# Performance work log

Hardware: AMD Instinct MI355X
Metric: run time of the kernel (lower is better)

Reference implementation:

```python
import jax, jax.numpy as jnp
import numpy as np

B, S, D, H = 32, 512, 512, 8
DF = D // H  # dim_feature = 64
NEG_INF = -1e32


def setup_inputs() -> dict:
    key = jax.random.key(0)
    ks = jax.random.split(key, 8)
    std = 1.0 / np.sqrt(D)  # xavier-ish scale for square linears
    return {
        "q": jax.random.normal(ks[0], (B, S, D), jnp.float32),
        "k": jax.random.normal(ks[1], (B, S, D), jnp.float32),
        "v": jax.random.normal(ks[2], (B, S, D), jnp.float32),
        "mask": jnp.tril(jnp.ones((S, S), jnp.int32))[None, None],  # causal AKT mask
        "zero_pad": 1,
        "question_difficulty_emb": jax.random.normal(ks[3], (B, S, S), jnp.float32) * 0.1,
        "Wk": jax.random.normal(ks[4], (D, D), jnp.float32) * std,
        "bk": jnp.zeros((D,), jnp.float32),
        "Wv": jax.random.normal(ks[5], (D, D), jnp.float32) * std,
        "bv": jnp.zeros((D,), jnp.float32),
        "Wo": jax.random.normal(ks[6], (D, D), jnp.float32) * std,
        "bo": jnp.zeros((D,), jnp.float32),
        "gammas": jax.random.normal(ks[7], (H, 1, 1), jnp.float32) * 0.1,
    }


def reference(q, k, v, mask, zero_pad, question_difficulty_emb, Wk, bk, Wv, bv, Wo, bo, gammas):
    bs = q.shape[0]

    def proj(x, W, b):
        # Linear then split heads: [B,S,D] -> [B,H,S,DF]
        return (x @ W.T + b).reshape(bs, -1, H, DF).transpose(0, 2, 1, 3)

    qh = proj(q, Wk, bk)  # key_query_same=True: q uses key_linear
    kh = proj(k, Wk, bk)
    vh = proj(v, Wv, bv)

    scores = jnp.einsum("bhqd,bhkd->bhqk", qh, kh) / jnp.sqrt(jnp.float32(DF))
    seqlen = scores.shape[-1]
    maskb = mask == 0  # [1,1,S,S]

    # --- distance-decay term (computed under no_grad in torch, detached) ---
    scores_ = jax.nn.softmax(jnp.where(maskb, NEG_INF, scores), axis=-1)
    scores_ = scores_ * mask.astype(scores.dtype)
    distcum = jnp.cumsum(scores_, axis=-1)                      # [B,H,S,S]
    disttot = jnp.sum(scores_, axis=-1, keepdims=True)          # [B,H,S,1]
    pos = jnp.abs(jnp.arange(seqlen)[None, :] - jnp.arange(seqlen)[:, None]).astype(scores.dtype)
    dist_scores = jnp.sqrt(jnp.clip((disttot - distcum) * pos[None, None], 0.0))
    dist_scores = jax.lax.stop_gradient(dist_scores)

    gamma = -jax.nn.softplus(gammas)[None]                      # [1,H,1,1]
    diff = jnp.exp(jax.nn.sigmoid(question_difficulty_emb))[:, None]  # [B,1,S,S]
    total_effect = jnp.clip(jnp.exp(dist_scores * gamma * diff), 1e-5, 1e5)

    scores = scores * total_effect
    scores = jax.nn.softmax(jnp.where(maskb, NEG_INF, scores), axis=-1)
    if zero_pad:
        scores = scores.at[:, :, 0, :].set(0.0)  # zero first query row
    scores = jnp.where(maskb, 0.0, scores)
    # dropout p=0 (eval) -> identity

    out = jnp.einsum("bhqk,bhkd->bhqd", scores, vh)
    concat = out.transpose(0, 2, 1, 3).reshape(bs, -1, D)
    return concat @ Wo.T + bo
```

## Files before the change

### kernel.cpp

```cpp
#include <hip/hip_runtime.h>

typedef unsigned short u16;
typedef __attribute__((ext_vector_type(8))) short short8;
typedef __attribute__((ext_vector_type(8))) _Float16 h8;
typedef __attribute__((ext_vector_type(4))) float f32x4;

__device__ __forceinline__ float b2f(u16 u) {
    return __uint_as_float(((unsigned int)u) << 16);
}
__device__ __forceinline__ u16 f2b(float f) {
    unsigned int x = __float_as_uint(f);
    return (u16)((x + 0x7FFFu + ((x >> 16) & 1u)) >> 16);
}
__device__ __forceinline__ float ldf(const void* p, size_t i, bool f32) {
    return f32 ? ((const float*)p)[i] : b2f(((const u16*)p)[i]);
}
__device__ __forceinline__ void stf(void* p, size_t i, bool f32, float v) {
    if (f32) ((float*)p)[i] = v; else ((u16*)p)[i] = f2b(v);
}
__device__ __forceinline__ float ex2(float x) {
    float r; asm("v_exp_f32 %0, %1" : "=v"(r) : "v"(x)); return r;
}
__device__ __forceinline__ float rsqf(float x) {
    float r; asm("v_rsq_f32 %0, %1" : "=v"(r) : "v"(x)); return r;
}

template<int CTRL, int RM, bool BC>
__device__ __forceinline__ float dppmov(float x) {
    return __uint_as_float((unsigned)__builtin_amdgcn_update_dpp(
        0, (int)__float_as_uint(x), CTRL, RM, 0xF, BC));
}
template<int LW>
__device__ __forceinline__ float seg_scan(float x, int ln) {
    if constexpr (LW >= 4) {
        x += dppmov<0x111, 0xF, true>(x);
        x += dppmov<0x112, 0xF, true>(x);
        x += dppmov<0x114, 0xF, true>(x);
        x += dppmov<0x118, 0xF, true>(x);
        if constexpr (LW >= 5)
            x += dppmov<0x142, 0xA, false>(x);
        if constexpr (LW >= 6)
            x += dppmov<0x143, 0xC, false>(x);
    } else {
        #pragma unroll
        for (int o = 1; o < (1 << LW); o <<= 1) {
            float u = __shfl_up(x, o, 1 << LW);
            if (ln >= o) x += u;
        }
    }
    return x;
}
template<int LW>
__device__ __forceinline__ float seg_bcast_last(float x) {
    if constexpr (LW == 6)
        return __uint_as_float((unsigned)__builtin_amdgcn_readlane(
            (int)__float_as_uint(x), 63));
    else
        return __shfl(x, (1 << LW) - 1, 1 << LW);
}

__device__ __forceinline__ void ldsld16(const void* g, void* l) {
    __builtin_amdgcn_global_load_lds(
        (const __attribute__((address_space(1))) unsigned int*)g,
        (__attribute__((address_space(3))) unsigned int*)l, 16, 0, 0);
}

__global__ void detect_f32(const u16* __restrict__ q, int* __restrict__ flag) {
    __shared__ int cw, cz;
    if (threadIdx.x == 0) { cw = 0; cz = 0; }
    __syncthreads();
    int w = 0, z = 0;
    for (int i = threadIdx.x; i < 4096; i += 256) {
        u16 u = q[i];
        int e = (u >> 7) & 0xFF;
        if (e >= 0xC8) w++;
        if (((i & 1) == 0) && u == 0) z++;
    }
    atomicAdd(&cw, w); atomicAdd(&cz, z);
    __syncthreads();
    if (threadIdx.x == 0) *flag = (cw > 8 || cz > 1024) ? 1 : 0;
}

__global__ __launch_bounds__(256) void cvt3(
    const void* __restrict__ s0, const void* __restrict__ s1,
    const void* __restrict__ s2, u16* __restrict__ d0, u16* __restrict__ d1,
    u16* __restrict__ d2, int n, const int* __restrict__ flag)
{
    const bool f32 = (*flag) != 0;
    const int z = blockIdx.z;
    const void* src = (z == 0) ? s0 : (z == 1) ? s1 : s2;
    u16* dst = (z == 0) ? d0 : (z == 1) ? d1 : d2;
    const int i = (blockIdx.x * 256 + threadIdx.x) * 8;
    if (i >= n) return;
    short8 o;
    if (f32) {
        const float4* s = (const float4*)((const float*)src + i);
        float4 v0 = s[0], v1 = s[1];
        o[0] = (short)f2b(v0.x); o[1] = (short)f2b(v0.y);
        o[2] = (short)f2b(v0.z); o[3] = (short)f2b(v0.w);
        o[4] = (short)f2b(v1.x); o[5] = (short)f2b(v1.y);
        o[6] = (short)f2b(v1.z); o[7] = (short)f2b(v1.w);
    } else {
        o = *(const short8*)((const u16*)src + i);
    }
    *(short8*)(dst + i) = o;
}

__global__ __launch_bounds__(256) void cvt4(
    const void* __restrict__ s0, const void* __restrict__ s1,
    const void* __restrict__ s2, const void* __restrict__ s3,
    u16* __restrict__ d0, u16* __restrict__ d1, u16* __restrict__ d2,
    _Float16* __restrict__ d3, int n, const int* __restrict__ flag)
{
    const bool f32 = (*flag) != 0;
    const int z = blockIdx.z;
    const int i = (blockIdx.x * 256 + threadIdx.x) * 8;
    if (i >= n) return;
    if (z == 3) {
        float x[8];
        if (f32) {
            const float4* s = (const float4*)((const float*)s3 + i);
            float4 v0 = s[0], v1 = s[1];
            x[0] = v0.x; x[1] = v0.y; x[2] = v0.z; x[3] = v0.w;
            x[4] = v1.x; x[5] = v1.y; x[6] = v1.z; x[7] = v1.w;
        } else {
            short8 v8 = *(const short8*)((const u16*)s3 + i);
            #pragma unroll
            for (int j = 0; j < 8; ++j) x[j] = b2f((u16)v8[j]);
        }
        h8 o;
        #pragma unroll
        for (int j = 0; j < 8; ++j) {
            float sig = __builtin_amdgcn_rcpf(1.f + __expf(-x[j]));
            o[j] = (_Float16)__expf(sig);
        }
        *(h8*)(d3 + i) = o;
        return;
    }
    const void* src = (z == 0) ? s0 : (z == 1) ? s1 : s2;
    u16* dst = (z == 0) ? d0 : (z == 1) ? d1 : d2;
    short8 o;
    if (f32) {
        const float4* s = (const float4*)((const float*)src + i);
        float4 v0 = s[0], v1 = s[1];
        o[0] = (short)f2b(v0.x); o[1] = (short)f2b(v0.y);
        o[2] = (short)f2b(v0.z); o[3] = (short)f2b(v0.w);
        o[4] = (short)f2b(v1.x); o[5] = (short)f2b(v1.y);
        o[6] = (short)f2b(v1.z); o[7] = (short)f2b(v1.w);
    } else {
        o = *(const short8*)((const u16*)src + i);
    }
    *(short8*)(dst + i) = o;
}

__global__ __launch_bounds__(256) void prep_diff(
    const void* __restrict__ qde, _Float16* __restrict__ diff, int n,
    const int* __restrict__ flag)
{
    const bool f32 = (*flag) != 0;
    const int i = (blockIdx.x * 256 + threadIdx.x) * 8;
    if (i >= n) return;
    float x[8];
    if (f32) {
        const float4* s = (const float4*)((const float*)qde + i);
        float4 v0 = s[0], v1 = s[1];
        x[0] = v0.x; x[1] = v0.y; x[2] = v0.z; x[3] = v0.w;
        x[4] = v1.x; x[5] = v1.y; x[6] = v1.z; x[7] = v1.w;
    } else {
        short8 v8 = *(const short8*)((const u16*)qde + i);
        #pragma unroll
        for (int j = 0; j < 8; ++j) x[j] = b2f((u16)v8[j]);
    }
    h8 o;
    #pragma unroll
    for (int j = 0; j < 8; ++j) {
        float sig = __builtin_amdgcn_rcpf(1.f + __expf(-x[j]));
        o[j] = (_Float16)__expf(sig);
    }
    *(h8*)(diff + i) = o;
}

#define BM 128
#define BN 128
#define BK 32

__device__ __forceinline__ void gemm_body(
    const u16* __restrict__ A, const u16* __restrict__ W,
    const void* __restrict__ bias, void* __restrict__ dst,
    bool f32, int mode, int bm, int bn, int M, int N, int K)
{
    __shared__ u16 As[BM * BK];
    __shared__ u16 Bs[BN * BK];
    const int t = threadIdx.x;
    const int w = t >> 6, l = t & 63, lq = l & 15, quad = l >> 4;
    const int wr = (w >> 1) * 64, wc = (w & 1) * 64;

    const int whalf = (w & 1) * 64;
    const u16* gsrc = (w < 2) ? A : W;
    const int  gbase = (w < 2) ? bm : bn;
    u16* lbase = (w < 2) ? As : Bs;

    f32x4 acc[4][4] = {};

    for (int k0 = 0; k0 < K; k0 += BK) {
        __syncthreads();
        #pragma unroll
        for (int c = 0; c < 4; ++c) {
            const int row = whalf + c * 16 + (l >> 2);
            ldsld16(gsrc + (size_t)(gbase + row) * K + k0 + (l & 3) * 8,
                    lbase + row * BK + (l & 3) * 8);
        }
        asm volatile("s_waitcnt vmcnt(0)" ::: "memory");
        __syncthreads();
        short8 af[4], bf[4];
        #pragma unroll
        for (int i = 0; i < 4; ++i)
            af[i] = *(const short8*)&As[(wr + i * 16 + lq) * BK + quad * 8];
        #pragma unroll
        for (int j = 0; j < 4; ++j)
            bf[j] = *(const short8*)&Bs[(wc + j * 16 + lq) * BK + quad * 8];
        #pragma unroll
        for (int i = 0; i < 4; ++i)
            #pragma unroll
            for (int j = 0; j < 4; ++j)
                acc[i][j] = __builtin_amdgcn_mfma_f32_16x16x32_bf16(
                    af[i], bf[j], acc[i][j], 0, 0, 0);
    }

    #pragma unroll
    for (int j = 0; j < 4; ++j) {
        const int n = bn + wc + j * 16 + lq;
        const float bb = ldf(bias, n, f32);
        #pragma unroll
        for (int i = 0; i < 4; ++i) {
            #pragma unroll
            for (int r = 0; r < 4; ++r) {
                const int m = bm + wr + i * 16 + quad * 4 + r;
                const float vout = acc[i][j][r] + bb;
                if (mode == 0) {
                    const int b = m >> 9, s = m & 511, hh = n >> 6, df = n & 63;
                    ((u16*)dst)[((((size_t)b * 8 + hh) * 512 + s) << 6) + df] = f2b(vout);
                } else if (mode == 2) {
                    const int b = m >> 9, s = m & 511, hh = n >> 6, df = n & 63;
                    _Float16 hv = (_Float16)vout;
                    ((u16*)dst)[((((size_t)b * 8 + hh) * 64 + df) << 9) + s] = *(const u16*)&hv;
                } else {
                    stf(dst, (size_t)m * N + n, f32, vout);
                }
            }
        }
    }
}

__global__ __launch_bounds__(256) void proj3(
    const u16* __restrict__ cq, const u16* __restrict__ ck,
    const u16* __restrict__ cv, const u16* __restrict__ cWk,
    const u16* __restrict__ cWv, const void* __restrict__ bk,
    const void* __restrict__ bv, u16* __restrict__ qh, u16* __restrict__ kh,
    u16* __restrict__ vt, const int* __restrict__ flag, int M, int N, int K)
{
    const int z = blockIdx.z;
    const u16* A = (z == 0) ? cq : (z == 1) ? ck : cv;
    const u16* W = (z < 2) ? cWk : cWv;
    const void* bias = (z < 2) ? bk : bv;
    void* dst = (z == 0) ? (void*)qh : (z == 1) ? (void*)kh : (void*)vt;
    gemm_body(A, W, bias, dst, (*flag) != 0, (z < 2) ? 0 : 2,
              blockIdx.y * BM, blockIdx.x * BN, M, N, K);
}

__global__ __launch_bounds__(256) void gemm_out(
    const u16* __restrict__ A, const u16* __restrict__ W,
    const void* __restrict__ bias, void* __restrict__ dst,
    const int* __restrict__ flag, int M, int N, int K)
{
    gemm_body(A, W, bias, dst, (*flag) != 0, 1,
              blockIdx.y * BM, blockIdx.x * BN, M, N, K);
}

#define QT  16
#define SRS 568
#define PRS 584

template<int LW>
__device__ __forceinline__ void phase2_impl(
    _Float16* __restrict__ s_h, u16* __restrict__ p_lds,
    const _Float16* __restrict__ diff, float gl2, int zp,
    int w, int l, int q0, int b)
{
    constexpr int W = 1 << LW;
    constexpr int R = 64 >> LW;
    constexpr int G = 16 / R;
    constexpr int NP = (G + 7) / 8;
    const int ln = l & (W - 1);
    const int seg = l >> LW;
    const int c0 = ln * 8;
    const int cm = c0 + 8 * (c0 >> 6);

    h8 dvv[NP], svv[NP];
    #pragma unroll
    for (int pp = 0; pp < NP; ++pp) {
        const int p = pp * 8 + w;
        if (G >= 8 || p < G) {
            const int row = p * R + seg;
            const int q = q0 + row;
            dvv[pp] = *(const h8*)(diff + ((size_t)b * 512 + q) * 512 + c0);
            svv[pp] = *(const h8*)(s_h + row * SRS + cm);
        }
    }

    #pragma unroll
    for (int pp = 0; pp < NP; ++pp) {
        const int p = pp * 8 + w;
        if (G >= 8 || p < G) {
            const int row = p * R + seg;
            const int q = q0 + row;
            const h8 dv = dvv[pp];
            const h8 sv16 = svv[pp];
            float sv[8], cs[8];
            float run = 0.f;
            #pragma unroll
            for (int j = 0; j < 8; ++j) {
                float s = (c0 + j <= q) ? (float)sv16[j] : -1e30f;
                sv[j] = s;
                float pe = ex2(s);
                run += pe; cs[j] = run;
            }
            const float incl = seg_scan<LW>(run, ln);
            const float ls   = seg_bcast_last<LW>(incl);
            const float t0   = ls - incl + run;
            const float grs  = gl2 * rsqf(ls);
            const float qf   = (float)(q - c0);
            float f8v[8]; float lf = 0.f;
            #pragma unroll
            for (int j = 0; j < 8; ++j) {
                float suf  = t0 - cs[j];
                float pos  = qf - (float)j;
                float ms   = fmaxf(suf * pos, 0.f);
                float dist = __builtin_amdgcn_sqrtf(ms);
                float a    = fmaxf(dist * grs * (float)dv[j], -16.609640474f);
                float eff  = ex2(a);
                float f    = ex2(sv[j] * eff);
                f8v[j] = f; lf += f;
            }
            if constexpr (LW == 3) {
                lf += __shfl_xor(lf, 4, 64);
                lf += __shfl_xor(lf, 2, 64);
                lf += __shfl_xor(lf, 1, 64);
            } else {
                lf = seg_bcast_last<LW>(seg_scan<LW>(lf, ln));
            }
            float inv2 = __builtin_amdgcn_rcpf(lf);
            if (zp && q == 0) inv2 = 0.f;
            h8 pb;
            #pragma unroll
            for (int j = 0; j < 8; ++j) pb[j] = (_Float16)(f8v[j] * inv2);
            *(h8*)((_Float16*)p_lds + row * PRS + cm) = pb;
        }
    }
}

__global__ __launch_bounds__(512) void akt_attn(
    const u16* __restrict__ qh, const u16* __restrict__ kh,
    const u16* __restrict__ vt, const _Float16* __restrict__ diff,
    const void* __restrict__ gammas, const int* __restrict__ zero_pad,
    const int* __restrict__ flag, u16* __restrict__ attn)
{
    __shared__ _Float16 s_h[QT * SRS];
    __shared__ u16      p_lds[QT * PRS];

    const int blk = blockIdx.x;
    const int h = blk & 7;
    const int i0 = blk >> 3;
    const int qt = 31 - (i0 & 31);
    const int b = i0 >> 5;

    const int q0 = qt * QT;
    const int t = threadIdx.x, w = t >> 6, l = t & 63;
    const int lq = l & 15, quad = l >> 4;
    const bool f32 = (*flag) != 0;
    const size_t bh = ((size_t)b * 8 + h) * 512;
    const int qmax = q0 + QT - 1;

    {
        const u16* qb = qh + (bh + q0) * 64;
        short8 af0 = *(const short8*)(qb + lq * 64 +      quad * 8);
        short8 af1 = *(const short8*)(qb + lq * 64 + 32 + quad * 8);
        const u16* kb = kh + bh * 64;
        const int KT = (q0 + QT + 127) >> 7;
        int n0 = w * 16;
        bool act = (n0 <= qmax);
        short8 bf0, bf1;
        if (act) {
            bf0 = *(const short8*)(kb + (size_t)(n0 + lq) * 64 +      quad * 8);
            bf1 = *(const short8*)(kb + (size_t)(n0 + lq) * 64 + 32 + quad * 8);
        }
        for (int kt = 0; kt < KT; ++kt) {
            const int n0n = (kt + 1) * 128 + w * 16;
            const bool actn = (kt + 1 < KT) && (n0n <= qmax);
            short8 nb0, nb1;
            if (actn) {
                nb0 = *(const short8*)(kb + (size_t)(n0n + lq) * 64 +      quad * 8);
                nb1 = *(const short8*)(kb + (size_t)(n0n + lq) * 64 + 32 + quad * 8);
            }
            if (act) {
                f32x4 acc = {0.f, 0.f, 0.f, 0.f};
                acc = __builtin_amdgcn_mfma_f32_16x16x32_bf16(af0, bf0, acc, 0, 0, 0);
                acc = __builtin_amdgcn_mfma_f32_16x16x32_bf16(af1, bf1, acc, 0, 0, 0);
                const int cm = n0 + lq + 8 * (n0 >> 6);
                #pragma unroll
                for (int r = 0; r < 4; ++r)
                    s_h[(quad * 4 + r) * SRS + cm] =
                        (_Float16)(acc[r] * 0.180336880f);
            }
            bf0 = nb0; bf1 = nb1; act = actn; n0 = n0n;
        }
    }
    __syncthreads();

    {
        const float g = ldf(gammas, h, f32);
        const float gl2 = -log1pf(expf(g)) * 1.4426950408889634f;
        const int zp = zero_pad[0];
        const int need = (qmax >> 3) + 1;
        if (need <= 8)
            phase2_impl<3>(s_h, p_lds, diff, gl2, zp, w, l, q0, b);
        else if (need <= 16)
            phase2_impl<4>(s_h, p_lds, diff, gl2, zp, w, l, q0, b);
        else if (need <= 32)
            phase2_impl<5>(s_h, p_lds, diff, gl2, zp, w, l, q0, b);
        else
            phase2_impl<6>(s_h, p_lds, diff, gl2, zp, w, l, q0, b);
    }
    __syncthreads();

    {
        const int g = w & 3;
        const int half = w >> 2;
        const int KS = (qmax >> 5) + 1;
        const _Float16* vb = (const _Float16*)vt +
            ((size_t)(b * 8 + h) * 64 + g * 16 + lq) * 512;
        const _Float16* prow = (const _Float16*)p_lds + lq * PRS;
        f32x4 oacc = {0.f, 0.f, 0.f, 0.f};
        for (int ks = half; ks < KS; ks += 2) {
            const int kb2 = ks * 32 + quad * 8;
            h8 pa = *(const h8*)(prow + kb2 + 8 * (kb2 >> 6));
            h8 vv = *(const h8*)(vb + kb2);
            oacc = __builtin_amdgcn_mfma_f32_16x16x32_f16(pa, vv, oacc, 0, 0, 0);
        }
        float* opart = (float*)s_h;
        if (half == 1) {
            #pragma unroll
            for (int r = 0; r < 4; ++r)
                opart[(g * 16 + quad * 4 + r) * 17 + lq] = oacc[r];
        }
        __syncthreads();
        if (half == 0) {
            const size_t ob = ((size_t)b * 512 + q0 + quad * 4) * 512 + h * 64 + g * 16 + lq;
            #pragma unroll
            for (int r = 0; r < 4; ++r)
                attn[ob + (size_t)r * 512] =
                    f2b(oacc[r] + opart[(g * 16 + quad * 4 + r) * 17 + lq]);
        }
    }
}

extern "C" void kernel_launch(void* const* d_in, const int* in_sizes, int n_in,
                              void* d_out, int out_size, void* d_ws, size_t ws_size,
                              hipStream_t stream) {
    const void* q   = d_in[0];
    const void* k   = d_in[1];
    const void* v   = d_in[2];
    const int*  zp  = (const int*)d_in[4];
    const void* qde = d_in[5];
    const void* Wk  = d_in[6];
    const void* bk  = d_in[7];
    const void* Wv  = d_in[8];
    const void* bv  = d_in[9];
    const void* Wo  = d_in[10];
    const void* bo  = d_in[11];
    const void* gam = d_in[12];

    const int M = 32 * 512, N = 512, K = 512;
    const int NBIG = M * K;
    const int NW = 512 * 512;

    char* ws = (char*)d_ws;
    int* flag = (int*)ws;
    const size_t SZB = (size_t)NBIG * 2;
    const size_t SZW = (size_t)NW * 2;
    u16* cWk  = (u16*)(ws + 1024);
    u16* cWv  = (u16*)(ws + 1024 + SZW);
    u16* cWo  = (u16*)(ws + 1024 + 2 * SZW);
    u16* cq   = (u16*)(ws + 1024 + 3 * SZW);
    u16* ck   = (u16*)(ws + 1024 + 3 * SZW + SZB);
    u16* cv   = (u16*)(ws + 1024 + 3 * SZW + 2 * SZB);
    u16* qh   = (u16*)(ws + 1024 + 3 * SZW + 3 * SZB);
    u16* kh   = (u16*)(ws + 1024 + 3 * SZW + 4 * SZB);
    u16* vt   = (u16*)(ws + 1024 + 3 * SZW + 5 * SZB);
    u16* attn = (u16*)(ws + 1024 + 3 * SZW + 6 * SZB);

    detect_f32<<<1, 256, 0, stream>>>((const u16*)q, flag);
    cvt3<<<dim3(NW / 2048, 1, 3), 256, 0, stream>>>(Wk, Wv, Wo, cWk, cWv, cWo, NW, flag);

    _Float16* diffb;
    const size_t need_ws = 1024 + 3 * SZW + 8 * SZB;
    if (ws_size >= need_ws) {
        diffb = (_Float16*)(ws + 1024 + 3 * SZW + 7 * SZB);
        cvt4<<<dim3(NBIG / 2048, 1, 4), 256, 0, stream>>>(
            q, k, v, qde, cq, ck, cv, diffb, NBIG, flag);
        proj3<<<dim3(N / BN, M / BM, 3), 256, 0, stream>>>(
            cq, ck, cv, cWk, cWv, bk, bv, qh, kh, vt, flag, M, N, K);
    } else {
        cvt3<<<dim3(NBIG / 2048, 1, 3), 256, 0, stream>>>(
            q, k, v, cq, ck, cv, NBIG, flag);
        proj3<<<dim3(N / BN, M / BM, 3), 256, 0, stream>>>(
            cq, ck, cv, cWk, cWv, bk, bv, qh, kh, vt, flag, M, N, K);
        diffb = (_Float16*)cq;
        prep_diff<<<dim3(NBIG / 2048), 256, 0, stream>>>(qde, diffb, NBIG, flag);
    }

    akt_attn<<<8192, 512, 0, stream>>>(qh, kh, vt, diffb, gam, zp, flag, attn);
    gemm_out<<<dim3(N / BN, M / BM), 256, 0, stream>>>(attn, cWo, bo, d_out, flag, M, N, K);
}
```

Baseline: 381.5 us.

## Shrink attention block to four waves, reuse score LDS for probabilities

The attention kernel now runs 256 threads (4 waves) per block instead of 512, with launch bounds asking for 8 blocks per CU. The separate probability LDS buffer is dropped and the softmax output is written in place over the score buffer, cutting LDS per block. The PV stage no longer splits K across two wave halves, which removes the partial-sum exchange and its extra barrier. The cost is more serial work per wave in every phase, and the phase-2 loads are no longer batched ahead of the compute.

```diff
diff --git a/kernel.cpp b/kernel.cpp
--- a/kernel.cpp
+++ b/kernel.cpp
@@ -279,43 +279,29 @@
 
 #define QT  16
 #define SRS 568
-#define PRS 584
 
 template<int LW>
 __device__ __forceinline__ void phase2_impl(
-    _Float16* __restrict__ s_h, u16* __restrict__ p_lds,
-    const _Float16* __restrict__ diff, float gl2, int zp,
-    int w, int l, int q0, int b)
+    _Float16* __restrict__ s_h, const _Float16* __restrict__ diff,
+    float gl2, int zp, int w, int l, int q0, int b)
 {
     constexpr int W = 1 << LW;
     constexpr int R = 64 >> LW;
     constexpr int G = 16 / R;
-    constexpr int NP = (G + 7) / 8;
+    constexpr int NP = (G + 3) / 4;
     const int ln = l & (W - 1);
     const int seg = l >> LW;
     const int c0 = ln * 8;
     const int cm = c0 + 8 * (c0 >> 6);
 
-    h8 dvv[NP], svv[NP];
     #pragma unroll
     for (int pp = 0; pp < NP; ++pp) {
-        const int p = pp * 8 + w;
-        if (G >= 8 || p < G) {
+        const int p = pp * 4 + w;
+        if (G >= 4 || p < G) {
             const int row = p * R + seg;
             const int q = q0 + row;
-            dvv[pp] = *(const h8*)(diff + ((size_t)b * 512 + q) * 512 + c0);
-            svv[pp] = *(const h8*)(s_h + row * SRS + cm);
-        }
-    }
-
-    #pragma unroll
-    for (int pp = 0; pp < NP; ++pp) {
-        const int p = pp * 8 + w;
-        if (G >= 8 || p < G) {
-            const int row = p * R + seg;
-            const int q = q0 + row;
-            const h8 dv = dvv[pp];
-            const h8 sv16 = svv[pp];
+            const h8 dv = *(const h8*)(diff + ((size_t)b * 512 + q) * 512 + c0);
+            const h8 sv16 = *(const h8*)(s_h + row * SRS + cm);
             float sv[8], cs[8];
             float run = 0.f;
             #pragma unroll
@@ -354,19 +340,18 @@
             h8 pb;
             #pragma unroll
             for (int j = 0; j < 8; ++j) pb[j] = (_Float16)(f8v[j] * inv2);
-            *(h8*)((_Float16*)p_lds + row * PRS + cm) = pb;
-        }
-    }
-}
-
-__global__ __launch_bounds__(512) void akt_attn(
+            *(h8*)(s_h + row * SRS + cm) = pb;
+        }
+    }
+}
+
+__global__ __launch_bounds__(256, 8) void akt_attn(
     const u16* __restrict__ qh, const u16* __restrict__ kh,
     const u16* __restrict__ vt, const _Float16* __restrict__ diff,
     const void* __restrict__ gammas, const int* __restrict__ zero_pad,
     const int* __restrict__ flag, u16* __restrict__ attn)
 {
     __shared__ _Float16 s_h[QT * SRS];
-    __shared__ u16      p_lds[QT * PRS];
 
     const int blk = blockIdx.x;
     const int h = blk & 7;
@@ -386,7 +371,7 @@
         short8 af0 = *(const short8*)(qb + lq * 64 +      quad * 8);
         short8 af1 = *(const short8*)(qb + lq * 64 + 32 + quad * 8);
         const u16* kb = kh + bh * 64;
-        const int KT = (q0 + QT + 127) >> 7;
+        const int KT = (q0 + QT + 63) >> 6;
         int n0 = w * 16;
         bool act = (n0 <= qmax);
         short8 bf0, bf1;
@@ -395,7 +380,7 @@
             bf1 = *(const short8*)(kb + (size_t)(n0 + lq) * 64 + 32 + quad * 8);
         }
         for (int kt = 0; kt < KT; ++kt) {
-            const int n0n = (kt + 1) * 128 + w * 16;
+            const int n0n = (kt + 1) * 64 + w * 16;
             const bool actn = (kt + 1 < KT) && (n0n <= qmax);
             short8 nb0, nb1;
             if (actn) {
@@ -423,44 +408,33 @@
         const int zp = zero_pad[0];
         const int need = (qmax >> 3) + 1;
         if (need <= 8)
-            phase2_impl<3>(s_h, p_lds, diff, gl2, zp, w, l, q0, b);
+            phase2_impl<3>(s_h, diff, gl2, zp, w, l, q0, b);
         else if (need <= 16)
-            phase2_impl<4>(s_h, p_lds, diff, gl2, zp, w, l, q0, b);
+            phase2_impl<4>(s_h, diff, gl2, zp, w, l, q0, b);
         else if (need <= 32)
-            phase2_impl<5>(s_h, p_lds, diff, gl2, zp, w, l, q0, b);
+            phase2_impl<5>(s_h, diff, gl2, zp, w, l, q0, b);
         else
-            phase2_impl<6>(s_h, p_lds, diff, gl2, zp, w, l, q0, b);
+            phase2_impl<6>(s_h, diff, gl2, zp, w, l, q0, b);
     }
     __syncthreads();
 
     {
-        const int g = w & 3;
-        const int half = w >> 2;
+        const int g = w;
         const int KS = (qmax >> 5) + 1;
         const _Float16* vb = (const _Float16*)vt +
             ((size_t)(b * 8 + h) * 64 + g * 16 + lq) * 512;
-        const _Float16* prow = (const _Float16*)p_lds + lq * PRS;
+        const _Float16* prow = s_h + lq * SRS;
         f32x4 oacc = {0.f, 0.f, 0.f, 0.f};
-        for (int ks = half; ks < KS; ks += 2) {
+        for (int ks = 0; ks < KS; ++ks) {
             const int kb2 = ks * 32 + quad * 8;
             h8 pa = *(const h8*)(prow + kb2 + 8 * (kb2 >> 6));
             h8 vv = *(const h8*)(vb + kb2);
             oacc = __builtin_amdgcn_mfma_f32_16x16x32_f16(pa, vv, oacc, 0, 0, 0);
         }
-        float* opart = (float*)s_h;
-        if (half == 1) {
-            #pragma unroll
-            for (int r = 0; r < 4; ++r)
-                opart[(g * 16 + quad * 4 + r) * 17 + lq] = oacc[r];
-        }
-        __syncthreads();
-        if (half == 0) {
-            const size_t ob = ((size_t)b * 512 + q0 + quad * 4) * 512 + h * 64 + g * 16 + lq;
-            #pragma unroll
-            for (int r = 0; r < 4; ++r)
-                attn[ob + (size_t)r * 512] =
-                    f2b(oacc[r] + opart[(g * 16 + quad * 4 + r) * 17 + lq]);
-        }
+        const size_t ob = ((size_t)b * 512 + q0 + quad * 4) * 512 + h * 64 + g * 16 + lq;
+        #pragma unroll
+        for (int r = 0; r < 4; ++r)
+            attn[ob + (size_t)r * 512] = f2b(oacc[r]);
     }
 }
 
@@ -519,6 +493,6 @@
         prep_diff<<<dim3(NBIG / 2048), 256, 0, stream>>>(qde, diffb, NBIG, flag);
     }
 
-    akt_attn<<<8192, 512, 0, stream>>>(qh, kh, vt, diffb, gam, zp, flag, attn);
+    akt_attn<<<8192, 256, 0, stream>>>(qh, kh, vt, diffb, gam, zp, flag, attn);
     gemm_out<<<dim3(N / BN, M / BM), 256, 0, stream>>>(attn, cWo, bo, d_out, flag, M, N, K);
 }
```

Measured after the change: 370.6 us. -2.8%, faster.
